# Performance work log

Hardware: AMD Instinct MI355X
Metric: run time of the kernel (lower is better)

## Reference

```python
import jax, jax.numpy as jnp
import numpy as np

OUT = 400          # resize target (tf.image.resize(img, [400, 400]))
THRESH = 0.7       # default threshold_value
B, H, W, C = 32, 512, 512, 3


def setup_inputs() -> dict:
    key = jax.random.key(0)
    k1, k2 = jax.random.split(key)
    image = jax.random.normal(k1, (B, H, W, C), dtype=jnp.float32)
    tensor = jax.random.uniform(k2, (B, H, W, 1), dtype=jnp.float32)
    return {"image": image, "tensor": tensor}


def _bounds(nz):
    # nz: bool [N]; first/last True index (tf.where(...)[0][0], [-1][0])
    n = nz.shape[0]
    first = jnp.argmax(nz).astype(jnp.int32)
    last = (n - 1 - jnp.argmax(nz[::-1])).astype(jnp.int32)
    return first, last


def _axis_coords(lo, hi, out):
    # TF2 bilinear resize: half-pixel centers, clamp into [0, size-1].
    # Crop is img[lo:hi] (exclusive hi, matching the TF slice semantics).
    size = (hi - lo).astype(jnp.float32)
    src = (jnp.arange(out, dtype=jnp.float32) + 0.5) * size / out - 0.5
    src = jnp.clip(src, 0.0, jnp.maximum(size - 1.0, 0.0))
    i0 = jnp.floor(src).astype(jnp.int32)
    i1 = jnp.minimum(i0 + 1, jnp.maximum(hi - lo - 1, 0))
    w = src - i0.astype(jnp.float32)
    return lo + i0, lo + i1, w  # absolute indices into the full image


def _crop_resize(img, msk):
    # img: [H, W, C]; msk: bool [H, W] == (tensor[..., 0] > THRESH)
    # rows: sum over axis=1 (tf sum_of_col), cols: sum over axis=0 (tf sum_of_row)
    left, right = _bounds(jnp.any(msk, axis=1))
    top, bot = _bounds(jnp.any(msk, axis=0))
    r0, r1, wr = _axis_coords(left, right, OUT)
    c0, c1, wc = _axis_coords(top, bot, OUT)
    a00 = img[r0[:, None], c0[None, :], :]
    a01 = img[r0[:, None], c1[None, :], :]
    a10 = img[r1[:, None], c0[None, :], :]
    a11 = img[r1[:, None], c1[None, :], :]
    wr_ = wr[:, None, None]
    wc_ = wc[None, :, None]
    top_i = a00 * (1.0 - wc_) + a01 * wc_
    bot_i = a10 * (1.0 - wc_) + a11 * wc_
    return top_i * (1.0 - wr_) + bot_i * wr_  # [OUT, OUT, C]


def reference(image, tensor):
    mask = tensor[..., 0] > THRESH
    return jax.vmap(_crop_resize)(image, mask)  # [B, 400, 400, C]
```

## Files before the change

### kernel.cpp

```cpp
#include <hip/hip_runtime.h>

#define OUTN 400
#define THRESH 0.7f
#define BB 32
#define HH 512
#define WW 512
#define CC 3
#define BIGI 0x7FFFFFFF

#define CHUNKS_PB 32
#define ROWS_PC   (HH / CHUNKS_PB)
#define PXPB      (OUTN * OUTN)
#define TPB       320
#define PXB       (TPB * 2)
#define BLKS_PB   (PXPB / PXB)
#define NXCD      8
#define RGRID     (BB * BLKS_PB)

typedef float vfloat4 __attribute__((ext_vector_type(4)));

__global__ void __launch_bounds__(256) border_kernel(
        const float* __restrict__ tensor,
        int4* __restrict__ part,
        int* __restrict__ flag) {
    const int b = blockIdx.x;
    const int t = threadIdx.x;
    const float* tb = tensor + (size_t)b * (HH * WW);

    bool r0any = false, r1any = false, c0any = false, c1any = false;

    if (t < 128) {
        vfloat4 v = ((const vfloat4*)tb)[t];
        r0any = (v.x > THRESH) | (v.y > THRESH) | (v.z > THRESH) | (v.w > THRESH);
    } else {
        vfloat4 v = ((const vfloat4*)(tb + (size_t)(HH - 1) * WW))[t - 128];
        r1any = (v.x > THRESH) | (v.y > THRESH) | (v.z > THRESH) | (v.w > THRESH);
    }
    {
        float a0 = tb[(size_t)t * WW];
        float a1 = tb[(size_t)(t + 256) * WW];
        c0any = (a0 > THRESH) | (a1 > THRESH);
        float b0 = tb[(size_t)t * WW + (WW - 1)];
        float b1 = tb[(size_t)(t + 256) * WW + (WW - 1)];
        c1any = (b0 > THRESH) | (b1 > THRESH);
    }

    __shared__ int s[4];
    if (t == 0) { s[0] = 0; s[1] = 0; s[2] = 0; s[3] = 0; }
    __syncthreads();
    bool a0 = __any(r0any), a1 = __any(r1any), a2 = __any(c0any), a3 = __any(c1any);
    if ((t & 63) == 0) {
        if (a0) atomicOr(&s[0], 1);
        if (a1) atomicOr(&s[1], 1);
        if (a2) atomicOr(&s[2], 1);
        if (a3) atomicOr(&s[3], 1);
    }
    __syncthreads();

    const bool full = s[0] && s[1] && s[2] && s[3];
    if (t == 0) flag[b] = full ? 1 : 0;
    if (full && t < CHUNKS_PB) {
        int4 fb; fb.x = 0; fb.y = HH - 1; fb.z = 0; fb.w = WW - 1;
        part[b * CHUNKS_PB + t] = fb;
    }
}

__global__ void __launch_bounds__(256) bounds_part_kernel(
        const float* __restrict__ tensor,
        const int* __restrict__ flag,
        int4* __restrict__ part) {
    const int task  = blockIdx.x;
    const int b     = task >> 5;
    const int chunk = task & 31;

    if (flag[b]) return;

    const vfloat4* base = (const vfloat4*)(tensor + (size_t)b * HH * WW
                                                  + (size_t)chunk * ROWS_PC * WW);

    int minR = BIGI, maxR = -1, minC = BIGI, maxC = -1;

    #pragma unroll
    for (int it = 0; it < 8; ++it) {
        int p = threadIdx.x + it * 256;
        vfloat4 v = __builtin_nontemporal_load(base + p);
        int row  = p >> 7;
        int col0 = (p & 127) * 4;
        int mask = (v.x > THRESH ? 1 : 0) | (v.y > THRESH ? 2 : 0)
                 | (v.z > THRESH ? 4 : 0) | (v.w > THRESH ? 8 : 0);
        if (mask) {
            minR = min(minR, row);
            maxR = max(maxR, row);
            minC = min(minC, col0 + __builtin_ctz(mask));
            maxC = max(maxC, col0 + (31 - __builtin_clz(mask)));
        }
    }

    #pragma unroll
    for (int off = 32; off > 0; off >>= 1) {
        minR = min(minR, __shfl_down(minR, off));
        maxR = max(maxR, __shfl_down(maxR, off));
        minC = min(minC, __shfl_down(minC, off));
        maxC = max(maxC, __shfl_down(maxC, off));
    }

    __shared__ int s[4];
    if (threadIdx.x == 0) { s[0] = BIGI; s[1] = -1; s[2] = BIGI; s[3] = -1; }
    __syncthreads();
    if ((threadIdx.x & 63) == 0) {
        atomicMin(&s[0], minR); atomicMax(&s[1], maxR);
        atomicMin(&s[2], minC); atomicMax(&s[3], maxC);
    }
    __syncthreads();
    if (threadIdx.x == 0) {
        int4 r;
        if (s[1] >= 0) {
            r.x = s[0] + chunk * ROWS_PC;
            r.y = s[1] + chunk * ROWS_PC;
            r.z = s[2];
            r.w = s[3];
        } else {
            r.x = BIGI; r.y = -1; r.z = BIGI; r.w = -1;
        }
        part[task] = r;
    }
}

__device__ inline int4 fold_bounds(const int4* __restrict__ part, int b, int lane) {
    int4 p = part[b * CHUNKS_PB + (lane & 31)];
    #pragma unroll
    for (int off = 1; off < 32; off <<= 1) {
        p.x = min(p.x, __shfl_xor(p.x, off));
        p.y = max(p.y, __shfl_xor(p.y, off));
        p.z = min(p.z, __shfl_xor(p.z, off));
        p.w = max(p.w, __shfl_xor(p.w, off));
    }
    if (p.y < 0) { p.x = 0; p.y = HH - 1; }
    if (p.w < 0) { p.z = 0; p.w = WW - 1; }
    return p;
}

__device__ inline void ld3(const float* __restrict__ p, float* d) {
    d[0] = p[0]; d[1] = p[1]; d[2] = p[2];
}

__global__ void __launch_bounds__(TPB) resize_kernel(
        const float* __restrict__ img,
        const int4* __restrict__ part,
        float* __restrict__ out) {
    const int logical = (blockIdx.x % NXCD) * (RGRID / NXCD) + blockIdx.x / NXCD;

    const int t    = threadIdx.x;
    const int b    = logical / BLKS_PB;
    const int rem  = (logical % BLKS_PB) * PXB + t * 2;
    const int lane = t & 63;

    int4 f = fold_bounds(part, b, lane);
    const int minR = f.x, maxR = f.y, minC = f.z, maxC = f.w;

    const int ocol = rem % OUTN;
    const int orow = rem / OUTN;

    float sizeR = (float)(maxR - minR);
    float srcR  = ((float)orow + 0.5f) * sizeR * (1.0f / OUTN) - 0.5f;
    srcR = fminf(fmaxf(srcR, 0.0f), fmaxf(sizeR - 1.0f, 0.0f));
    int   i0 = (int)floorf(srcR);
    int   i1 = min(i0 + 1, max(maxR - minR - 1, 0));
    float wr = srcR - (float)i0;
    const int ro0 = (minR + i0) * (WW * CC);
    const int ro1 = (minR + i1) * (WW * CC);

    const float sizeC  = (float)(maxC - minC);
    const float hiClip = fmaxf(sizeC - 1.0f, 0.0f);
    const int   jmax   = max(maxC - minC - 1, 0);

    float srcC0 = ((float)ocol + 0.5f) * sizeC * (1.0f / OUTN) - 0.5f;
    srcC0 = fminf(fmaxf(srcC0, 0.0f), hiClip);
    int   j00 = (int)floorf(srcC0);
    int   j01 = min(j00 + 1, jmax);
    float wc0 = srcC0 - (float)j00;
    const int c00 = (minC + j00) * CC, c01 = (minC + j01) * CC;

    float srcC1 = ((float)ocol + 1.5f) * sizeC * (1.0f / OUTN) - 0.5f;
    srcC1 = fminf(fmaxf(srcC1, 0.0f), hiClip);
    int   j10 = (int)floorf(srcC1);
    int   j11 = min(j10 + 1, jmax);
    float wc1 = srcC1 - (float)j10;
    const int c10 = (minC + j10) * CC, c11 = (minC + j11) * CC;

    const float* __restrict__ ib = img + (size_t)b * (HH * WW * CC);

    float a00[3], a01[3], a10[3], a11[3];
    float d00[3], d01[3], d10[3], d11[3];
    ld3(ib + ro0 + c00, a00);
    ld3(ib + ro0 + c01, a01);
    ld3(ib + ro1 + c00, a10);
    ld3(ib + ro1 + c01, a11);
    ld3(ib + ro0 + c10, d00);
    ld3(ib + ro0 + c11, d01);
    ld3(ib + ro1 + c10, d10);
    ld3(ib + ro1 + c11, d11);

    float res[6];
    {
        float omc = 1.0f - wc0, omr = 1.0f - wr;
        #pragma unroll
        for (int ch = 0; ch < CC; ++ch) {
            float top = a00[ch] * omc + a01[ch] * wc0;
            float bot = a10[ch] * omc + a11[ch] * wc0;
            res[ch] = top * omr + bot * wr;
        }
        omc = 1.0f - wc1;
        #pragma unroll
        for (int ch = 0; ch < CC; ++ch) {
            float top = d00[ch] * omc + d01[ch] * wc1;
            float bot = d10[ch] * omc + d11[ch] * wc1;
            res[3 + ch] = top * omr + bot * wr;
        }
    }

    float* o = out + ((size_t)b * PXPB + (size_t)rem) * CC;
    #pragma unroll
    for (int i = 0; i < 6; ++i)
        __builtin_nontemporal_store(res[i], o + i);
}

extern "C" void kernel_launch(void* const* d_in, const int* in_sizes, int n_in,
                              void* d_out, int out_size, void* d_ws, size_t ws_size,
                              hipStream_t stream) {
    const float* image  = (const float*)d_in[0];
    const float* tensor = (const float*)d_in[1];
    float* out  = (float*)d_out;
    int4*  part = (int4*)d_ws;
    int*   flag = (int*)(part + BB * CHUNKS_PB);

    hipLaunchKernelGGL(border_kernel, dim3(BB), dim3(256), 0, stream,
                       tensor, part, flag);

    hipLaunchKernelGGL(bounds_part_kernel, dim3(BB * CHUNKS_PB), dim3(256), 0, stream,
                       tensor, flag, part);

    hipLaunchKernelGGL(resize_kernel, dim3(RGRID), dim3(TPB), 0, stream,
                       image, part, out);
}
```

Before: 38.55 us.

## Merge border check and bounds scan into one per-batch kernel

Fuses the border early-exit kernel and the chunked bounds-partial kernel into a single kernel with one block per batch. That block either writes full bounds at once or scans the whole mask serially with 256 threads. The resize kernel now reads one precomputed int4 per batch instead of folding 32 partials with shuffles. This removes a kernel launch and the fold work. The cost is that the fallback scan has far less parallelism, since only 32 blocks cover the whole tensor.

```diff
diff --git a/kernel.cpp b/kernel.cpp
--- a/kernel.cpp
+++ b/kernel.cpp
@@ -8,8 +8,6 @@
 #define CC 3
 #define BIGI 0x7FFFFFFF
 
-#define CHUNKS_PB 32
-#define ROWS_PC   (HH / CHUNKS_PB)
 #define PXPB      (OUTN * OUTN)
 #define TPB       320
 #define PXB       (TPB * 2)
@@ -19,10 +17,9 @@
 
 typedef float vfloat4 __attribute__((ext_vector_type(4)));
 
-__global__ void __launch_bounds__(256) border_kernel(
+__global__ void __launch_bounds__(256) bounds_final_kernel(
         const float* __restrict__ tensor,
-        int4* __restrict__ part,
-        int* __restrict__ flag) {
+        int4* __restrict__ finals) {
     const int b = blockIdx.x;
     const int t = threadIdx.x;
     const float* tb = tensor + (size_t)b * (HH * WW);
@@ -57,32 +54,17 @@
     }
     __syncthreads();
 
-    const bool full = s[0] && s[1] && s[2] && s[3];
-    if (t == 0) flag[b] = full ? 1 : 0;
-    if (full && t < CHUNKS_PB) {
-        int4 fb; fb.x = 0; fb.y = HH - 1; fb.z = 0; fb.w = WW - 1;
-        part[b * CHUNKS_PB + t] = fb;
-    }
-}
-
-__global__ void __launch_bounds__(256) bounds_part_kernel(
-        const float* __restrict__ tensor,
-        const int* __restrict__ flag,
-        int4* __restrict__ part) {
-    const int task  = blockIdx.x;
-    const int b     = task >> 5;
-    const int chunk = task & 31;
-
-    if (flag[b]) return;
-
-    const vfloat4* base = (const vfloat4*)(tensor + (size_t)b * HH * WW
-                                                  + (size_t)chunk * ROWS_PC * WW);
+    if (s[0] && s[1] && s[2] && s[3]) {
+        if (t == 0) {
+            int4 f; f.x = 0; f.y = HH - 1; f.z = 0; f.w = WW - 1;
+            finals[b] = f;
+        }
+        return;
+    }
 
     int minR = BIGI, maxR = -1, minC = BIGI, maxC = -1;
-
-    #pragma unroll
-    for (int it = 0; it < 8; ++it) {
-        int p = threadIdx.x + it * 256;
+    const vfloat4* base = (const vfloat4*)tb;
+    for (int p = t; p < (HH * WW) / 4; p += 256) {
         vfloat4 v = __builtin_nontemporal_load(base + p);
         int row  = p >> 7;
         int col0 = (p & 127) * 4;
@@ -104,40 +86,20 @@
         maxC = max(maxC, __shfl_down(maxC, off));
     }
 
-    __shared__ int s[4];
-    if (threadIdx.x == 0) { s[0] = BIGI; s[1] = -1; s[2] = BIGI; s[3] = -1; }
-    __syncthreads();
-    if ((threadIdx.x & 63) == 0) {
-        atomicMin(&s[0], minR); atomicMax(&s[1], maxR);
-        atomicMin(&s[2], minC); atomicMax(&s[3], maxC);
-    }
-    __syncthreads();
-    if (threadIdx.x == 0) {
-        int4 r;
-        if (s[1] >= 0) {
-            r.x = s[0] + chunk * ROWS_PC;
-            r.y = s[1] + chunk * ROWS_PC;
-            r.z = s[2];
-            r.w = s[3];
-        } else {
-            r.x = BIGI; r.y = -1; r.z = BIGI; r.w = -1;
-        }
-        part[task] = r;
-    }
-}
-
-__device__ inline int4 fold_bounds(const int4* __restrict__ part, int b, int lane) {
-    int4 p = part[b * CHUNKS_PB + (lane & 31)];
-    #pragma unroll
-    for (int off = 1; off < 32; off <<= 1) {
-        p.x = min(p.x, __shfl_xor(p.x, off));
-        p.y = max(p.y, __shfl_xor(p.y, off));
-        p.z = min(p.z, __shfl_xor(p.z, off));
-        p.w = max(p.w, __shfl_xor(p.w, off));
-    }
-    if (p.y < 0) { p.x = 0; p.y = HH - 1; }
-    if (p.w < 0) { p.z = 0; p.w = WW - 1; }
-    return p;
+    __shared__ int r[4];
+    if (t == 0) { r[0] = BIGI; r[1] = -1; r[2] = BIGI; r[3] = -1; }
+    __syncthreads();
+    if ((t & 63) == 0) {
+        atomicMin(&r[0], minR); atomicMax(&r[1], maxR);
+        atomicMin(&r[2], minC); atomicMax(&r[3], maxC);
+    }
+    __syncthreads();
+    if (t == 0) {
+        int4 f;
+        if (r[1] >= 0) { f.x = r[0]; f.y = r[1]; } else { f.x = 0; f.y = HH - 1; }
+        if (r[3] >= 0) { f.z = r[2]; f.w = r[3]; } else { f.z = 0; f.w = WW - 1; }
+        finals[b] = f;
+    }
 }
 
 __device__ inline void ld3(const float* __restrict__ p, float* d) {
@@ -146,16 +108,15 @@
 
 __global__ void __launch_bounds__(TPB) resize_kernel(
         const float* __restrict__ img,
-        const int4* __restrict__ part,
+        const int4* __restrict__ finals,
         float* __restrict__ out) {
     const int logical = (blockIdx.x % NXCD) * (RGRID / NXCD) + blockIdx.x / NXCD;
 
     const int t    = threadIdx.x;
     const int b    = logical / BLKS_PB;
     const int rem  = (logical % BLKS_PB) * PXB + t * 2;
-    const int lane = t & 63;
-
-    int4 f = fold_bounds(part, b, lane);
+
+    const int4 f = finals[b];
     const int minR = f.x, maxR = f.y, minC = f.z, maxC = f.w;
 
     const int ocol = rem % OUTN;
@@ -230,16 +191,12 @@
                               hipStream_t stream) {
     const float* image  = (const float*)d_in[0];
     const float* tensor = (const float*)d_in[1];
-    float* out  = (float*)d_out;
-    int4*  part = (int4*)d_ws;
-    int*   flag = (int*)(part + BB * CHUNKS_PB);
-
-    hipLaunchKernelGGL(border_kernel, dim3(BB), dim3(256), 0, stream,
-                       tensor, part, flag);
-
-    hipLaunchKernelGGL(bounds_part_kernel, dim3(BB * CHUNKS_PB), dim3(256), 0, stream,
-                       tensor, flag, part);
+    float* out    = (float*)d_out;
+    int4*  finals = (int4*)d_ws;
+
+    hipLaunchKernelGGL(bounds_final_kernel, dim3(BB), dim3(256), 0, stream,
+                       tensor, finals);
 
     hipLaunchKernelGGL(resize_kernel, dim3(RGRID), dim3(TPB), 0, stream,
-                       image, part, out);
-}
+                       image, finals, out);
+}
```

New measurement: 34.69 us. 1.11x faster.
